# Kernel tuning notes

Measured on AMD Instinct MI355X. Metric: run time of the kernel, lower is better.

The kernel has to match this reference:

```python
import jax, jax.numpy as jnp
import numpy as np

HEADS = 8
DIM_HEAD = 64
QUERY_DIM = 512
CONTEXT_DIM = 768
INNER = HEADS * DIM_HEAD  # 512


def setup_inputs() -> dict:
    key = jax.random.key(0)
    ks = jax.random.split(key, 8)
    s = lambda fan_in: 1.0 / np.sqrt(fan_in)
    return {
        "x": jax.random.normal(ks[0], (16, 4096, QUERY_DIM), dtype=jnp.float32),
        "context": jax.random.normal(ks[1], (16, 77, CONTEXT_DIM), dtype=jnp.float32),
        "ln_gamma": jnp.ones((QUERY_DIM,), dtype=jnp.float32),
        "ln_beta": jnp.zeros((QUERY_DIM,), dtype=jnp.float32),
        "Wq": jax.random.uniform(ks[2], (QUERY_DIM, INNER), jnp.float32, -s(QUERY_DIM), s(QUERY_DIM)),
        "Wk": jax.random.uniform(ks[3], (CONTEXT_DIM, INNER), jnp.float32, -s(CONTEXT_DIM), s(CONTEXT_DIM)),
        "Wv": jax.random.uniform(ks[4], (CONTEXT_DIM, INNER), jnp.float32, -s(CONTEXT_DIM), s(CONTEXT_DIM)),
        "Wo": jax.random.uniform(ks[5], (INNER, QUERY_DIM), jnp.float32, -s(INNER), s(INNER)),
        "bo": jax.random.uniform(ks[6], (QUERY_DIM,), jnp.float32, -s(INNER), s(INNER)),
    }


def _layernorm(x, gamma, beta, eps=1e-5):
    mu = jnp.mean(x, axis=-1, keepdims=True)
    var = jnp.mean((x - mu) ** 2, axis=-1, keepdims=True)
    return (x - mu) * jax.lax.rsqrt(var + eps) * gamma + beta


def reference(x, context, ln_gamma, ln_beta, Wq, Wk, Wv, Wo, bo):
    B, N, D = x.shape
    scale = DIM_HEAD ** -0.5
    h = _layernorm(x, ln_gamma, ln_beta)
    # project then split heads: [B, H, S, d]
    q = (h @ Wq).reshape(B, N, HEADS, DIM_HEAD).transpose(0, 2, 1, 3)
    M = context.shape[1]
    k = (context @ Wk).reshape(B, M, HEADS, DIM_HEAD).transpose(0, 2, 1, 3)
    v = (context @ Wv).reshape(B, M, HEADS, DIM_HEAD).transpose(0, 2, 1, 3)
    scores = jnp.einsum("bhnd,bhmd->bhnm", q, k) * scale
    attn = jax.nn.softmax(scores, axis=-1)
    out = jnp.einsum("bhnm,bhmd->bhnd", attn, v)  # [B,H,N,d]
    out = out.transpose(0, 2, 1, 3).reshape(B, N, INNER)
    return x + out @ Wo + bo
```

## Files before the change

kernel.cpp:

```cpp
#include <hip/hip_runtime.h>


#define DQ 512
#define DC 768
#define MCTX 77
#define MPAD 96
#define DH 64

typedef __attribute__((ext_vector_type(8))) short bf16x8;
typedef __attribute__((ext_vector_type(4))) short s16x4;
typedef __attribute__((ext_vector_type(4))) float f32x4;
typedef __attribute__((ext_vector_type(16))) float f32x16;

__device__ __forceinline__ short f2bf(float f) {
    unsigned u = __builtin_bit_cast(unsigned, f);
    u = (u + 0x7FFFu + ((u >> 16) & 1u)) >> 16;
    return (short)u;
}
__device__ __forceinline__ unsigned cvtpk(float lo, float hi) {
    unsigned r;
    asm("v_cvt_pk_bf16_f32 %0, %1, %2" : "=v"(r) : "v"(lo), "v"(hi));
    return r;
}

#define SWZ(row, byte) ((byte) ^ (((row) & 7) << 4))
#define MFMA(a, b, c) __builtin_amdgcn_mfma_f32_16x16x32_bf16((a), (b), (c), 0, 0, 0)
#define MFMA32(a, b, c) __builtin_amdgcn_mfma_f32_32x32x16_bf16((a), (b), (c), 0, 0, 0)

__global__ void prep_weights(const float* __restrict__ Wq, const float* __restrict__ Wk,
                             const float* __restrict__ Wv, const float* __restrict__ Wo,
                             short* __restrict__ WqF, short* __restrict__ WkT,
                             short* __restrict__ WvT, short* __restrict__ WoF) {
    __shared__ float t[32][33];
    int bid = blockIdx.x;
    if (bid < 256) {
        const float* src = (bid < 128) ? Wq : Wo;
        short* dst = (bid < 128) ? WqF : WoF;
        int vb = bid & 127;
        int idx = vb * 256 + threadIdx.x;
        int lane = idx & 63;
        int chunk = idx >> 6;
        int tt = chunk % 16, ks = chunk / 16;
        int n = tt * 32 + (lane & 31);
        int k0 = ks * 16 + (lane >> 5) * 8;
        bf16x8 v;
#pragma unroll
        for (int j = 0; j < 8; ++j) v[j] = f2bf(src[(size_t)(k0 + j) * 512 + n]);
        *(bf16x8*)(dst + (size_t)idx * 8) = v;
    } else {
        const float* src = (bid < 640) ? Wk : Wv;
        short* dst = (bid < 640) ? WkT : WvT;
        int vb = (bid - 256) % 384;
        int tn = vb % 16, tk = vb / 16;
        int tx = threadIdx.x & 31, ty = threadIdx.x >> 5;
#pragma unroll
        for (int i = 0; i < 32; i += 8)
            t[ty + i][tx] = src[(size_t)(tk * 32 + ty + i) * 512 + tn * 32 + tx];
        __syncthreads();
#pragma unroll
        for (int i = 0; i < 32; i += 8)
            dst[(size_t)(tn * 32 + ty + i) * 768 + tk * 32 + tx] = f2bf(t[tx][ty + i]);
    }
}

__global__ __launch_bounds__(256, 1) void kv_proj(const float* __restrict__ ctxin,
                                                  const short* __restrict__ WkT,
                                                  const short* __restrict__ WvT,
                                                  short* __restrict__ Kb,
                                                  short* __restrict__ VbT) {
    int b = blockIdx.x >> 2;
    int kv = (blockIdx.x >> 1) & 1;
    int half = blockIdx.x & 1;
    const short* WT = kv ? WvT : WkT;

    __shared__ short A[48 * 768];
    const int tid = threadIdx.x;
    const int lane = tid & 63, wv = tid >> 6;
    const int l15 = lane & 15, l4 = lane >> 4;

#pragma unroll
    for (int it = 0; it < 36; ++it) {
        int id = it * 256 + tid;
        int row = id / 192, col = (id % 192) * 4;
        int gctx = half * 48 + row;
        float4 v = make_float4(0.f, 0.f, 0.f, 0.f);
        if (gctx < MCTX)
            v = ((const float4*)(ctxin + ((size_t)(b * MCTX + gctx)) * DC))[id % 192];
        s16x4 s4;
        s4[0] = f2bf(v.x); s4[1] = f2bf(v.y); s4[2] = f2bf(v.z); s4[3] = f2bf(v.w);
        *(s16x4*)((char*)A + row * 1536 + SWZ(row, col * 2)) = s4;
    }
    __syncthreads();

    f32x4 zf = {0.f, 0.f, 0.f, 0.f};
    f32x4 acc[3][8];
#pragma unroll
    for (int m = 0; m < 3; ++m)
#pragma unroll
        for (int nb = 0; nb < 8; ++nb) acc[m][nb] = zf;

    for (int ks = 0; ks < 24; ++ks) {
        bf16x8 bb[8], aa[3];
#pragma unroll
        for (int nb = 0; nb < 8; ++nb) {
            int n = wv * 128 + nb * 16 + l15;
            bb[nb] = *(const bf16x8*)((const char*)WT + (size_t)n * 1536 + ks * 64 + l4 * 16);
        }
#pragma unroll
        for (int m = 0; m < 3; ++m) {
            int row = m * 16 + l15;
            aa[m] = *(const bf16x8*)((char*)A + row * 1536 + SWZ(row, ks * 64 + l4 * 16));
        }
#pragma unroll
        for (int nb = 0; nb < 8; ++nb)
#pragma unroll
            for (int m = 0; m < 3; ++m) acc[m][nb] = MFMA(aa[m], bb[nb], acc[m][nb]);
    }

    if (kv == 0) {
#pragma unroll
        for (int m = 0; m < 3; ++m)
#pragma unroll
            for (int nb = 0; nb < 8; ++nb)
#pragma unroll
                for (int r = 0; r < 4; ++r) {
                    int ctxi = half * 48 + m * 16 + l4 * 4 + r;
                    int col = wv * 128 + nb * 16 + l15;
                    Kb[((size_t)(b * MPAD + ctxi)) * 512 + col] = f2bf(acc[m][nb][r]);
                }
    } else {
#pragma unroll
        for (int m = 0; m < 3; ++m)
#pragma unroll
            for (int nb = 0; nb < 8; ++nb)
#pragma unroll
                for (int r = 0; r < 4; ++r) {
                    int ctxi = half * 48 + m * 16 + l4 * 4 + r;
                    int col = wv * 128 + nb * 16 + l15;
                    VbT[((size_t)(b * 512 + col)) * MPAD + ctxi] = f2bf(acc[m][nb][r]);
                }
    }
}

__global__ __launch_bounds__(512, 4) void fused_attn(
    const float* __restrict__ x, const float* __restrict__ gamma,
    const float* __restrict__ beta, const short* __restrict__ WqF,
    const short* __restrict__ WoF, const short* __restrict__ Kb,
    const short* __restrict__ VbT, const float* __restrict__ bo,
    float* __restrict__ out) {
    __shared__ short A[64 * 512];

    const int tid = threadIdx.x;
    const int lane = tid & 63, wv = tid >> 6;
    const int l15 = lane & 15, l4 = lane >> 4;
    const int l31 = lane & 31, hi5 = lane >> 5;
    const int swz = (blockIdx.x & 7) * 128 + (blockIdx.x >> 3);
    const int b = swz >> 6;
    const size_t rowbase = (size_t)swz * 64;
    const int cb = wv * 64;

    {
        float g[8], be[8];
        float4 g0 = ((const float4*)gamma)[lane * 2], g1 = ((const float4*)gamma)[lane * 2 + 1];
        float4 b0 = ((const float4*)beta)[lane * 2], b1 = ((const float4*)beta)[lane * 2 + 1];
        g[0] = g0.x; g[1] = g0.y; g[2] = g0.z; g[3] = g0.w;
        g[4] = g1.x; g[5] = g1.y; g[6] = g1.z; g[7] = g1.w;
        be[0] = b0.x; be[1] = b0.y; be[2] = b0.z; be[3] = b0.w;
        be[4] = b1.x; be[5] = b1.y; be[6] = b1.z; be[7] = b1.w;
#pragma unroll 1
        for (int g4 = 0; g4 < 2; ++g4) {
            float4 v0[4], v1[4];
#pragma unroll
            for (int j = 0; j < 4; ++j) {
                int row = wv * 8 + g4 * 4 + j;
                const float4* xp = (const float4*)(x + (rowbase + row) * DQ);
                v0[j] = xp[lane * 2];
                v1[j] = xp[lane * 2 + 1];
            }
#pragma unroll
            for (int j = 0; j < 4; ++j) {
                int row = wv * 8 + g4 * 4 + j;
                float vv[8] = {v0[j].x, v0[j].y, v0[j].z, v0[j].w,
                               v1[j].x, v1[j].y, v1[j].z, v1[j].w};
                float s = 0.f, s2 = 0.f;
#pragma unroll
                for (int i = 0; i < 8; ++i) { s += vv[i]; s2 = fmaf(vv[i], vv[i], s2); }
#pragma unroll
                for (int m = 1; m < 64; m <<= 1) {
                    s += __shfl_xor(s, m);
                    s2 += __shfl_xor(s2, m);
                }
                float mu = s * (1.f / 512.f);
                float var = s2 * (1.f / 512.f) - mu * mu;
                float rs = rsqrtf(var + 1e-5f);
                float hn[8];
#pragma unroll
                for (int i = 0; i < 8; ++i) hn[i] = (vv[i] - mu) * rs * g[i] + be[i];
                uint4 hv = make_uint4(cvtpk(hn[0], hn[1]), cvtpk(hn[2], hn[3]),
                                      cvtpk(hn[4], hn[5]), cvtpk(hn[6], hn[7]));
                *(uint4*)((char*)A + row * 1024 + SWZ(row, lane * 16)) = hv;
            }
        }
    }

    f32x4 zf = {0.f, 0.f, 0.f, 0.f};

#define LDWF(dst, W, ks)                                                                   \
    _Pragma("unroll") for (int tt = 0; tt < 2; ++tt) {                                     \
        (dst)[tt] = *(const bf16x8*)((W) +                                                 \
            (size_t)((((ks)*16 + wv * 2 + tt) * 64 + lane)) * 8);                          \
    }
#define LDT32(dst, ks)                                                                     \
    _Pragma("unroll") for (int tt = 0; tt < 2; ++tt) {                                     \
        int row = tt * 32 + l31;                                                           \
        (dst)[tt] = *(const bf16x8*)((char*)A + row * 1024 +                               \
                                     SWZ(row, (ks)*32 + hi5 * 16));                        \
    }
#define GSTEP_Q(W, ACC, WBASE, kk)                                                         \
    {                                                                                      \
        bf16x8 hb[2];                                                                      \
        LDT32(hb, (kk));                                                                   \
        _Pragma("unroll") for (int mt = 0; mt < 2; ++mt)                                   \
            _Pragma("unroll") for (int nt = 0; nt < 2; ++nt)                               \
                ACC[mt][nt] = MFMA32((W)[mt], hb[nt], ACC[mt][nt]);                        \
        LDWF((W), (WBASE), (kk) + 4);                                                      \
    }
#define GSTEP_Q_NR(W, ACC, kk)                                                             \
    {                                                                                      \
        bf16x8 hb[2];                                                                      \
        LDT32(hb, (kk));                                                                   \
        _Pragma("unroll") for (int mt = 0; mt < 2; ++mt)                                   \
            _Pragma("unroll") for (int nt = 0; nt < 2; ++nt)                               \
                ACC[mt][nt] = MFMA32((W)[mt], hb[nt], ACC[mt][nt]);                        \
    }
#define GSTEP_O(W, ACC, WBASE, kk)                                                         \
    {                                                                                      \
        bf16x8 hb[2];                                                                      \
        LDT32(hb, (kk));                                                                   \
        _Pragma("unroll") for (int mt = 0; mt < 2; ++mt)                                   \
            _Pragma("unroll") for (int ct = 0; ct < 2; ++ct)                               \
                ACC[mt][ct] = MFMA32(hb[mt], (W)[ct], ACC[mt][ct]);                        \
        LDWF((W), (WBASE), (kk) + 4);                                                      \
    }
#define GSTEP_O_NR(W, ACC, kk)                                                             \
    {                                                                                      \
        bf16x8 hb[2];                                                                      \
        LDT32(hb, (kk));                                                                   \
        _Pragma("unroll") for (int mt = 0; mt < 2; ++mt)                                   \
            _Pragma("unroll") for (int ct = 0; ct < 2; ++ct)                               \
                ACC[mt][ct] = MFMA32(hb[mt], (W)[ct], ACC[mt][ct]);                        \
    }

    {
        bf16x8 w0[2], w1[2], w2[2], w3[2];
        LDWF(w0, WqF, 0);
        LDWF(w1, WqF, 1);
        LDWF(w2, WqF, 2);
        LDWF(w3, WqF, 3);
        __syncthreads();

        f32x16 qa[2][2];
#pragma unroll
        for (int mt = 0; mt < 2; ++mt)
#pragma unroll
            for (int nt = 0; nt < 2; ++nt)
#pragma unroll
                for (int i = 0; i < 16; ++i) qa[mt][nt][i] = 0.f;

#pragma unroll 1
        for (int ks = 0; ks < 28; ks += 4) {
            GSTEP_Q(w0, qa, WqF, ks)
            GSTEP_Q(w1, qa, WqF, ks + 1)
            GSTEP_Q(w2, qa, WqF, ks + 2)
            GSTEP_Q(w3, qa, WqF, ks + 3)
        }
        GSTEP_Q_NR(w0, qa, 28)
        GSTEP_Q_NR(w1, qa, 29)
        GSTEP_Q_NR(w2, qa, 30)
        GSTEP_Q_NR(w3, qa, 31)
        __syncthreads();

#pragma unroll
        for (int mt = 0; mt < 2; ++mt)
#pragma unroll
            for (int nt = 0; nt < 2; ++nt)
#pragma unroll
                for (int g = 0; g < 4; ++g) {
                    uint2 qv = make_uint2(
                        cvtpk(qa[mt][nt][g * 4] * 0.125f, qa[mt][nt][g * 4 + 1] * 0.125f),
                        cvtpk(qa[mt][nt][g * 4 + 2] * 0.125f, qa[mt][nt][g * 4 + 3] * 0.125f));
                    int row = nt * 32 + l31;
                    int colb = (cb + mt * 32 + 8 * g + 4 * hi5) * 2;
                    *(uint2*)((char*)A + row * 1024 + SWZ(row, colb)) = qv;
                }
    }

    {
        const int srcA = ((l4 & 1) << 5) + l15;
        const int srcB = srcA + 16;
        const bool hi = (l4 >> 1) != 0;

#pragma unroll 1
        for (int rp = 0; rp < 4; ++rp) {
            bf16x8 qf0, qf1;
            {
                int qrow = rp * 16 + l15;
                qf0 = *(const bf16x8*)((char*)A + qrow * 1024 + SWZ(qrow, cb * 2 + l4 * 16));
                qf1 = *(const bf16x8*)((char*)A + qrow * 1024 + SWZ(qrow, cb * 2 + 64 + l4 * 16));
            }
            f32x4 sc[5];
            __builtin_amdgcn_s_setprio(1);
#pragma unroll
            for (int f = 0; f < 5; ++f) {
                bf16x8 k0 = *(const bf16x8*)(Kb + ((size_t)(b * MPAD + f * 16 + l15)) * 512 +
                                             cb + l4 * 8);
                bf16x8 k1 = *(const bf16x8*)(Kb + ((size_t)(b * MPAD + f * 16 + l15)) * 512 +
                                             cb + 32 + l4 * 8);
                sc[f] = MFMA(k0, qf0, zf);
                sc[f] = MFMA(k1, qf1, sc[f]);
            }
            __builtin_amdgcn_s_setprio(0);
            float m = -1e30f;
#pragma unroll
            for (int f = 0; f < 5; ++f)
#pragma unroll
                for (int r = 0; r < 4; ++r) {
                    float v = sc[f][r];
                    if (f == 4 && (64 + l4 * 4 + r) >= MCTX) v = -1e30f;
                    sc[f][r] = v;
                    m = fmaxf(m, v);
                }
            m = fmaxf(m, __shfl_xor(m, 16));
            m = fmaxf(m, __shfl_xor(m, 32));
            float s = 0.f;
#pragma unroll
            for (int f = 0; f < 5; ++f)
#pragma unroll
                for (int r = 0; r < 4; ++r) {
                    float p = __expf(sc[f][r] - m);
                    sc[f][r] = p;
                    s += p;
                }
            s += __shfl_xor(s, 16);
            s += __shfl_xor(s, 32);
            float inv = 1.f / s;
            unsigned pk[6][2];
#pragma unroll
            for (int f = 0; f < 5; ++f) {
                pk[f][0] = cvtpk(sc[f][0] * inv, sc[f][1] * inv);
                pk[f][1] = cvtpk(sc[f][2] * inv, sc[f][3] * inv);
            }
            pk[5][0] = 0; pk[5][1] = 0;

            f32x4 ov[4];
#pragma unroll
            for (int nb = 0; nb < 4; ++nb) ov[nb] = zf;
#pragma unroll
            for (int ks = 0; ks < 3; ++ks) {
                unsigned aL0 = __shfl((int)pk[2 * ks][0], srcA);
                unsigned aL1 = __shfl((int)pk[2 * ks][1], srcA);
                unsigned aH0 = __shfl((int)pk[2 * ks + 1][0], srcA);
                unsigned aH1 = __shfl((int)pk[2 * ks + 1][1], srcA);
                unsigned bL0 = __shfl((int)pk[2 * ks][0], srcB);
                unsigned bL1 = __shfl((int)pk[2 * ks][1], srcB);
                unsigned bH0 = __shfl((int)pk[2 * ks + 1][0], srcB);
                unsigned bH1 = __shfl((int)pk[2 * ks + 1][1], srcB);
                unsigned paw[4];
                paw[0] = hi ? aH0 : aL0;
                paw[1] = hi ? aH1 : aL1;
                paw[2] = hi ? bH0 : bL0;
                paw[3] = hi ? bH1 : bL1;
                bf16x8 ap = __builtin_bit_cast(bf16x8, paw);
                __builtin_amdgcn_s_setprio(1);
#pragma unroll
                for (int nb = 0; nb < 4; ++nb) {
                    bf16x8 bv = *(const bf16x8*)(VbT +
                                                 ((size_t)(b * 512 + cb + nb * 16 + l15)) * MPAD +
                                                 ks * 32 + l4 * 8);
                    ov[nb] = MFMA(bv, ap, ov[nb]);
                }
                __builtin_amdgcn_s_setprio(0);
            }
#pragma unroll
            for (int nb = 0; nb < 4; ++nb) {
                uint2 av = make_uint2(cvtpk(ov[nb][0], ov[nb][1]),
                                      cvtpk(ov[nb][2], ov[nb][3]));
                int row = rp * 16 + l15;
                int colb = (cb + nb * 16 + l4 * 4) * 2;
                *(uint2*)((char*)A + row * 1024 + SWZ(row, colb)) = av;
            }
        }
    }

    {
        bf16x8 w0[2], w1[2], w2[2], w3[2];
        LDWF(w0, WoF, 0);
        LDWF(w1, WoF, 1);
        LDWF(w2, WoF, 2);
        LDWF(w3, WoF, 3);
        __syncthreads();

        f32x16 oa[2][2];
#pragma unroll
        for (int mt = 0; mt < 2; ++mt)
#pragma unroll
            for (int ct = 0; ct < 2; ++ct)
#pragma unroll
                for (int i = 0; i < 16; ++i) oa[mt][ct][i] = 0.f;

#pragma unroll 1
        for (int ks = 0; ks < 28; ks += 4) {
            GSTEP_O(w0, oa, WoF, ks)
            GSTEP_O(w1, oa, WoF, ks + 1)
            GSTEP_O(w2, oa, WoF, ks + 2)
            GSTEP_O(w3, oa, WoF, ks + 3)
        }
        GSTEP_O_NR(w0, oa, 28)
        GSTEP_O_NR(w1, oa, 29)
        GSTEP_O_NR(w2, oa, 30)
        GSTEP_O_NR(w3, oa, 31)

#pragma unroll
        for (int mt = 0; mt < 2; ++mt)
#pragma unroll
            for (int ct = 0; ct < 2; ++ct) {
                int col = cb + ct * 32 + l31;
                float bov = bo[col];
                float xv[16];
#pragma unroll
                for (int rg = 0; rg < 16; ++rg) {
                    int row = mt * 32 + (rg & 3) + 8 * (rg >> 2) + 4 * hi5;
                    xv[rg] = x[(rowbase + row) * DQ + col];
                }
#pragma unroll
                for (int rg = 0; rg < 16; ++rg) {
                    int row = mt * 32 + (rg & 3) + 8 * (rg >> 2) + 4 * hi5;
                    size_t gi = (rowbase + row) * DQ + col;
                    out[gi] = xv[rg] + oa[mt][ct][rg] + bov;
                }
            }
    }
}

extern "C" void kernel_launch(void* const* d_in, const int* in_sizes, int n_in,
                              void* d_out, int out_size, void* d_ws, size_t ws_size,
                              hipStream_t stream) {
    const float* x = (const float*)d_in[0];
    const float* ctx = (const float*)d_in[1];
    const float* gamma = (const float*)d_in[2];
    const float* beta = (const float*)d_in[3];
    const float* Wq = (const float*)d_in[4];
    const float* Wk = (const float*)d_in[5];
    const float* Wv = (const float*)d_in[6];
    const float* Wo = (const float*)d_in[7];
    const float* bo = (const float*)d_in[8];
    float* out = (float*)d_out;

    char* ws = (char*)d_ws;
    short* WqF = (short*)(ws + 0);
    short* WkT = (short*)(ws + 524288);
    short* WvT = (short*)(ws + 1310720);
    short* WoF = (short*)(ws + 2097152);
    short* Kb = (short*)(ws + 2621440);
    short* VbT = (short*)(ws + 4194304);

    prep_weights<<<1024, 256, 0, stream>>>(Wq, Wk, Wv, Wo, WqF, WkT, WvT, WoF);
    kv_proj<<<64, 256, 0, stream>>>(ctx, WkT, WvT, Kb, VbT);
    fused_attn<<<1024, 512, 0, stream>>>(x, gamma, beta, WqF, WoF, Kb, VbT, bo, out);
}
```

Baseline: 195.7 us.

## Process 128 rows per block with 16 waves to halve weight reloads

Each fused attention block now covers 128 query rows with 1024 threads instead of 64 rows with 512 threads. Each wave owns one 32-column slice of the Q and output projections across all 128 rows, so every weight fragment loaded from global memory is reused across twice as many rows and total weight traffic is halved. The attention stage splits the 16 waves into two groups of row pairs, and the Wo prefetch is moved ahead of the attention stage. The cost is double the LDS per block (128 KB), which allows fewer resident blocks per CU and larger synchronisation groups, and there are only 512 blocks to fill the GPU.

```diff
diff --git a/kernel.cpp b/kernel.cpp
--- a/kernel.cpp
+++ b/kernel.cpp
@@ -6,6 +6,7 @@
 #define MCTX 77
 #define MPAD 96
 #define DH 64
+#define ROWS 128
 
 typedef __attribute__((ext_vector_type(8))) short bf16x8;
 typedef __attribute__((ext_vector_type(4))) short s16x4;
@@ -142,22 +143,21 @@
     }
 }
 
-__global__ __launch_bounds__(512, 4) void fused_attn(
+__global__ __launch_bounds__(1024, 4) void fused_attn(
     const float* __restrict__ x, const float* __restrict__ gamma,
     const float* __restrict__ beta, const short* __restrict__ WqF,
     const short* __restrict__ WoF, const short* __restrict__ Kb,
     const short* __restrict__ VbT, const float* __restrict__ bo,
     float* __restrict__ out) {
-    __shared__ short A[64 * 512];
+    __shared__ short A[ROWS * 512];
 
     const int tid = threadIdx.x;
-    const int lane = tid & 63, wv = tid >> 6;
+    const int lane = tid & 63, w16 = tid >> 6;
     const int l15 = lane & 15, l4 = lane >> 4;
     const int l31 = lane & 31, hi5 = lane >> 5;
-    const int swz = (blockIdx.x & 7) * 128 + (blockIdx.x >> 3);
-    const int b = swz >> 6;
-    const size_t rowbase = (size_t)swz * 64;
-    const int cb = wv * 64;
+    const int swz = (blockIdx.x & 7) * 64 + (blockIdx.x >> 3);
+    const int b = swz >> 5;
+    const size_t rowbase = (size_t)swz * ROWS;
 
     {
         float g[8], be[8];
@@ -172,14 +172,14 @@
             float4 v0[4], v1[4];
 #pragma unroll
             for (int j = 0; j < 4; ++j) {
-                int row = wv * 8 + g4 * 4 + j;
+                int row = w16 * 8 + g4 * 4 + j;
                 const float4* xp = (const float4*)(x + (rowbase + row) * DQ);
                 v0[j] = xp[lane * 2];
                 v1[j] = xp[lane * 2 + 1];
             }
 #pragma unroll
             for (int j = 0; j < 4; ++j) {
-                int row = wv * 8 + g4 * 4 + j;
+                int row = w16 * 8 + g4 * 4 + j;
                 float vv[8] = {v0[j].x, v0[j].y, v0[j].z, v0[j].w,
                                v1[j].x, v1[j].y, v1[j].z, v1[j].w};
                 float s = 0.f, s2 = 0.f;
@@ -205,67 +205,58 @@
 
     f32x4 zf = {0.f, 0.f, 0.f, 0.f};
 
-#define LDWF(dst, W, ks)                                                                   \
-    _Pragma("unroll") for (int tt = 0; tt < 2; ++tt) {                                     \
-        (dst)[tt] = *(const bf16x8*)((W) +                                                 \
-            (size_t)((((ks)*16 + wv * 2 + tt) * 64 + lane)) * 8);                          \
-    }
-#define LDT32(dst, ks)                                                                     \
-    _Pragma("unroll") for (int tt = 0; tt < 2; ++tt) {                                     \
-        int row = tt * 32 + l31;                                                           \
-        (dst)[tt] = *(const bf16x8*)((char*)A + row * 1024 +                               \
+#define LDWF1(dst, W, ks)                                                                  \
+    (dst) = *(const bf16x8*)((W) + (size_t)((((ks)*16 + w16) * 64 + lane)) * 8);
+#define LDT128(dst, ks)                                                                    \
+    _Pragma("unroll") for (int nt = 0; nt < 4; ++nt) {                                     \
+        int row = nt * 32 + l31;                                                           \
+        (dst)[nt] = *(const bf16x8*)((char*)A + row * 1024 +                               \
                                      SWZ(row, (ks)*32 + hi5 * 16));                        \
     }
 #define GSTEP_Q(W, ACC, WBASE, kk)                                                         \
     {                                                                                      \
-        bf16x8 hb[2];                                                                      \
-        LDT32(hb, (kk));                                                                   \
-        _Pragma("unroll") for (int mt = 0; mt < 2; ++mt)                                   \
-            _Pragma("unroll") for (int nt = 0; nt < 2; ++nt)                               \
-                ACC[mt][nt] = MFMA32((W)[mt], hb[nt], ACC[mt][nt]);                        \
-        LDWF((W), (WBASE), (kk) + 4);                                                      \
+        bf16x8 hb[4];                                                                      \
+        LDT128(hb, (kk));                                                                  \
+        _Pragma("unroll") for (int nt = 0; nt < 4; ++nt)                                   \
+            ACC[nt] = MFMA32((W), hb[nt], ACC[nt]);                                        \
+        LDWF1((W), (WBASE), (kk) + 4);                                                     \
     }
 #define GSTEP_Q_NR(W, ACC, kk)                                                             \
     {                                                                                      \
-        bf16x8 hb[2];                                                                      \
-        LDT32(hb, (kk));                                                                   \
-        _Pragma("unroll") for (int mt = 0; mt < 2; ++mt)                                   \
-            _Pragma("unroll") for (int nt = 0; nt < 2; ++nt)                               \
-                ACC[mt][nt] = MFMA32((W)[mt], hb[nt], ACC[mt][nt]);                        \
+        bf16x8 hb[4];                                                                      \
+        LDT128(hb, (kk));                                                                  \
+        _Pragma("unroll") for (int nt = 0; nt < 4; ++nt)                                   \
+            ACC[nt] = MFMA32((W), hb[nt], ACC[nt]);                                        \
     }
 #define GSTEP_O(W, ACC, WBASE, kk)                                                         \
     {                                                                                      \
-        bf16x8 hb[2];                                                                      \
-        LDT32(hb, (kk));                                                                   \
-        _Pragma("unroll") for (int mt = 0; mt < 2; ++mt)                                   \
-            _Pragma("unroll") for (int ct = 0; ct < 2; ++ct)                               \
-                ACC[mt][ct] = MFMA32(hb[mt], (W)[ct], ACC[mt][ct]);                        \
-        LDWF((W), (WBASE), (kk) + 4);                                                      \
+        bf16x8 hb[4];                                                                      \
+        LDT128(hb, (kk));                                                                  \
+        _Pragma("unroll") for (int mt = 0; mt < 4; ++mt)                                   \
+            ACC[mt] = MFMA32(hb[mt], (W), ACC[mt]);                                        \
+        LDWF1((W), (WBASE), (kk) + 4);                                                     \
     }
 #define GSTEP_O_NR(W, ACC, kk)                                                             \
     {                                                                                      \
-        bf16x8 hb[2];                                                                      \
-        LDT32(hb, (kk));                                                                   \
-        _Pragma("unroll") for (int mt = 0; mt < 2; ++mt)                                   \
-            _Pragma("unroll") for (int ct = 0; ct < 2; ++ct)                               \
-                ACC[mt][ct] = MFMA32(hb[mt], (W)[ct], ACC[mt][ct]);                        \
+        bf16x8 hb[4];                                                                      \
+        LDT128(hb, (kk));                                                                  \
+        _Pragma("unroll") for (int mt = 0; mt < 4; ++mt)                                   \
+            ACC[mt] = MFMA32(hb[mt], (W), ACC[mt]);                                        \
     }
 
     {
-        bf16x8 w0[2], w1[2], w2[2], w3[2];
-        LDWF(w0, WqF, 0);
-        LDWF(w1, WqF, 1);
-        LDWF(w2, WqF, 2);
-        LDWF(w3, WqF, 3);
+        bf16x8 w0, w1, w2, w3;
+        LDWF1(w0, WqF, 0);
+        LDWF1(w1, WqF, 1);
+        LDWF1(w2, WqF, 2);
+        LDWF1(w3, WqF, 3);
         __syncthreads();
 
-        f32x16 qa[2][2];
-#pragma unroll
-        for (int mt = 0; mt < 2; ++mt)
-#pragma unroll
-            for (int nt = 0; nt < 2; ++nt)
-#pragma unroll
-                for (int i = 0; i < 16; ++i) qa[mt][nt][i] = 0.f;
+        f32x16 qa[4];
+#pragma unroll
+        for (int nt = 0; nt < 4; ++nt)
+#pragma unroll
+            for (int i = 0; i < 16; ++i) qa[nt][i] = 0.f;
 
 #pragma unroll 1
         for (int ks = 0; ks < 28; ks += 4) {
@@ -281,27 +272,35 @@
         __syncthreads();
 
 #pragma unroll
-        for (int mt = 0; mt < 2; ++mt)
-#pragma unroll
-            for (int nt = 0; nt < 2; ++nt)
-#pragma unroll
-                for (int g = 0; g < 4; ++g) {
-                    uint2 qv = make_uint2(
-                        cvtpk(qa[mt][nt][g * 4] * 0.125f, qa[mt][nt][g * 4 + 1] * 0.125f),
-                        cvtpk(qa[mt][nt][g * 4 + 2] * 0.125f, qa[mt][nt][g * 4 + 3] * 0.125f));
-                    int row = nt * 32 + l31;
-                    int colb = (cb + mt * 32 + 8 * g + 4 * hi5) * 2;
-                    *(uint2*)((char*)A + row * 1024 + SWZ(row, colb)) = qv;
-                }
-    }
+        for (int nt = 0; nt < 4; ++nt)
+#pragma unroll
+            for (int g = 0; g < 4; ++g) {
+                uint2 qv = make_uint2(
+                    cvtpk(qa[nt][g * 4] * 0.125f, qa[nt][g * 4 + 1] * 0.125f),
+                    cvtpk(qa[nt][g * 4 + 2] * 0.125f, qa[nt][g * 4 + 3] * 0.125f));
+                int row = nt * 32 + l31;
+                int colb = (w16 * 32 + 8 * g + 4 * hi5) * 2;
+                *(uint2*)((char*)A + row * 1024 + SWZ(row, colb)) = qv;
+            }
+        __syncthreads();
+    }
+
+    bf16x8 wo0, wo1, wo2, wo3;
+    LDWF1(wo0, WoF, 0);
+    LDWF1(wo1, WoF, 1);
+    LDWF1(wo2, WoF, 2);
+    LDWF1(wo3, WoF, 3);
 
     {
+        const int cb = (w16 & 7) * 64;
+        const int rpb = (w16 >> 3) * 4;
         const int srcA = ((l4 & 1) << 5) + l15;
         const int srcB = srcA + 16;
         const bool hi = (l4 >> 1) != 0;
 
 #pragma unroll 1
-        for (int rp = 0; rp < 4; ++rp) {
+        for (int rp2 = 0; rp2 < 4; ++rp2) {
+            const int rp = rpb + rp2;
             bf16x8 qf0, qf1;
             {
                 int qrow = rp * 16 + l15;
@@ -393,39 +392,31 @@
     }
 
     {
-        bf16x8 w0[2], w1[2], w2[2], w3[2];
-        LDWF(w0, WoF, 0);
-        LDWF(w1, WoF, 1);
-        LDWF(w2, WoF, 2);
-        LDWF(w3, WoF, 3);
         __syncthreads();
 
-        f32x16 oa[2][2];
-#pragma unroll
-        for (int mt = 0; mt < 2; ++mt)
-#pragma unroll
-            for (int ct = 0; ct < 2; ++ct)
-#pragma unroll
-                for (int i = 0; i < 16; ++i) oa[mt][ct][i] = 0.f;
+        f32x16 oa[4];
+#pragma unroll
+        for (int mt = 0; mt < 4; ++mt)
+#pragma unroll
+            for (int i = 0; i < 16; ++i) oa[mt][i] = 0.f;
 
 #pragma unroll 1
         for (int ks = 0; ks < 28; ks += 4) {
-            GSTEP_O(w0, oa, WoF, ks)
-            GSTEP_O(w1, oa, WoF, ks + 1)
-            GSTEP_O(w2, oa, WoF, ks + 2)
-            GSTEP_O(w3, oa, WoF, ks + 3)
-        }
-        GSTEP_O_NR(w0, oa, 28)
-        GSTEP_O_NR(w1, oa, 29)
-        GSTEP_O_NR(w2, oa, 30)
-        GSTEP_O_NR(w3, oa, 31)
-
-#pragma unroll
-        for (int mt = 0; mt < 2; ++mt)
-#pragma unroll
-            for (int ct = 0; ct < 2; ++ct) {
-                int col = cb + ct * 32 + l31;
-                float bov = bo[col];
+            GSTEP_O(wo0, oa, WoF, ks)
+            GSTEP_O(wo1, oa, WoF, ks + 1)
+            GSTEP_O(wo2, oa, WoF, ks + 2)
+            GSTEP_O(wo3, oa, WoF, ks + 3)
+        }
+        GSTEP_O_NR(wo0, oa, 28)
+        GSTEP_O_NR(wo1, oa, 29)
+        GSTEP_O_NR(wo2, oa, 30)
+        GSTEP_O_NR(wo3, oa, 31)
+
+        {
+            int col = w16 * 32 + l31;
+            float bov = bo[col];
+#pragma unroll
+            for (int mt = 0; mt < 4; ++mt) {
                 float xv[16];
 #pragma unroll
                 for (int rg = 0; rg < 16; ++rg) {
@@ -436,9 +427,10 @@
                 for (int rg = 0; rg < 16; ++rg) {
                     int row = mt * 32 + (rg & 3) + 8 * (rg >> 2) + 4 * hi5;
                     size_t gi = (rowbase + row) * DQ + col;
-                    out[gi] = xv[rg] + oa[mt][ct][rg] + bov;
-                }
-            }
+                    out[gi] = xv[rg] + oa[mt][rg] + bov;
+                }
+            }
+        }
     }
 }
 
@@ -466,5 +458,5 @@
 
     prep_weights<<<1024, 256, 0, stream>>>(Wq, Wk, Wv, Wo, WqF, WkT, WvT, WoF);
     kv_proj<<<64, 256, 0, stream>>>(ctx, WkT, WvT, Kb, VbT);
-    fused_attn<<<1024, 512, 0, stream>>>(x, gamma, beta, WqF, WoF, Kb, VbT, bo, out);
-}
+    fused_attn<<<512, 1024, 0, stream>>>(x, gamma, beta, WqF, WoF, Kb, VbT, bo, out);
+}
```

After: 190.7 us. 1.03x faster.

## Retile Q and O projections to 32-row by 128-col warp tiles

Applied to the files above, without the earlier changes.

Changes the per-warp tiling of the Q and output projection GEMMs from a 64x64 tile (2x2 of 32x32 MFMAs) to a 32x128 tile (one A row-block times four weight column-blocks). This halves the LDS reads of activations per MFMA, doubles the per-warp weight fragment loads from global memory, and shortens weight prefetch to two stages. The Q writeback to LDS now happens before the barrier rather than after it, which removes one synchronisation, and the setprio scope in the PV loop is widened to cover all k-steps. The trade-off is more global and L2 weight traffic per block in exchange for less LDS pressure.

```diff
diff --git a/kernel.cpp b/kernel.cpp
--- a/kernel.cpp
+++ b/kernel.cpp
@@ -154,10 +154,10 @@
     const int lane = tid & 63, wv = tid >> 6;
     const int l15 = lane & 15, l4 = lane >> 4;
     const int l31 = lane & 31, hi5 = lane >> 5;
+    const int rg = wv >> 2, cg = wv & 3;
     const int swz = (blockIdx.x & 7) * 128 + (blockIdx.x >> 3);
     const int b = swz >> 6;
     const size_t rowbase = (size_t)swz * 64;
-    const int cb = wv * 64;
 
     {
         float g[8], be[8];
@@ -205,97 +205,84 @@
 
     f32x4 zf = {0.f, 0.f, 0.f, 0.f};
 
-#define LDWF(dst, W, ks)                                                                   \
-    _Pragma("unroll") for (int tt = 0; tt < 2; ++tt) {                                     \
+#define LDWF4(dst, W, ks)                                                                  \
+    _Pragma("unroll") for (int tt = 0; tt < 4; ++tt) {                                     \
         (dst)[tt] = *(const bf16x8*)((W) +                                                 \
-            (size_t)((((ks)*16 + wv * 2 + tt) * 64 + lane)) * 8);                          \
-    }
-#define LDT32(dst, ks)                                                                     \
-    _Pragma("unroll") for (int tt = 0; tt < 2; ++tt) {                                     \
-        int row = tt * 32 + l31;                                                           \
-        (dst)[tt] = *(const bf16x8*)((char*)A + row * 1024 +                               \
-                                     SWZ(row, (ks)*32 + hi5 * 16));                        \
-    }
-#define GSTEP_Q(W, ACC, WBASE, kk)                                                         \
+            (size_t)((((ks)*16 + cg * 4 + tt) * 64 + lane)) * 8);                          \
+    }
+#define LDT1R(dst, ks)                                                                     \
     {                                                                                      \
-        bf16x8 hb[2];                                                                      \
-        LDT32(hb, (kk));                                                                   \
-        _Pragma("unroll") for (int mt = 0; mt < 2; ++mt)                                   \
-            _Pragma("unroll") for (int nt = 0; nt < 2; ++nt)                               \
-                ACC[mt][nt] = MFMA32((W)[mt], hb[nt], ACC[mt][nt]);                        \
-        LDWF((W), (WBASE), (kk) + 4);                                                      \
-    }
-#define GSTEP_Q_NR(W, ACC, kk)                                                             \
+        int row_ = rg * 32 + l31;                                                          \
+        (dst) = *(const bf16x8*)((char*)A + row_ * 1024 +                                  \
+                                 SWZ(row_, (ks)*32 + hi5 * 16));                           \
+    }
+#define GSTEPQ(W, kk)                                                                      \
     {                                                                                      \
-        bf16x8 hb[2];                                                                      \
-        LDT32(hb, (kk));                                                                   \
-        _Pragma("unroll") for (int mt = 0; mt < 2; ++mt)                                   \
-            _Pragma("unroll") for (int nt = 0; nt < 2; ++nt)                               \
-                ACC[mt][nt] = MFMA32((W)[mt], hb[nt], ACC[mt][nt]);                        \
-    }
-#define GSTEP_O(W, ACC, WBASE, kk)                                                         \
+        bf16x8 hb;                                                                         \
+        LDT1R(hb, (kk));                                                                   \
+        _Pragma("unroll") for (int ct = 0; ct < 4; ++ct)                                   \
+            qa[ct] = MFMA32((W)[ct], hb, qa[ct]);                                          \
+        LDWF4((W), WqF, (kk) + 2);                                                         \
+    }
+#define GSTEPQ_NR(W, kk)                                                                   \
     {                                                                                      \
-        bf16x8 hb[2];                                                                      \
-        LDT32(hb, (kk));                                                                   \
-        _Pragma("unroll") for (int mt = 0; mt < 2; ++mt)                                   \
-            _Pragma("unroll") for (int ct = 0; ct < 2; ++ct)                               \
-                ACC[mt][ct] = MFMA32(hb[mt], (W)[ct], ACC[mt][ct]);                        \
-        LDWF((W), (WBASE), (kk) + 4);                                                      \
-    }
-#define GSTEP_O_NR(W, ACC, kk)                                                             \
+        bf16x8 hb;                                                                         \
+        LDT1R(hb, (kk));                                                                   \
+        _Pragma("unroll") for (int ct = 0; ct < 4; ++ct)                                   \
+            qa[ct] = MFMA32((W)[ct], hb, qa[ct]);                                          \
+    }
+#define GSTEPO(W, kk)                                                                      \
     {                                                                                      \
-        bf16x8 hb[2];                                                                      \
-        LDT32(hb, (kk));                                                                   \
-        _Pragma("unroll") for (int mt = 0; mt < 2; ++mt)                                   \
-            _Pragma("unroll") for (int ct = 0; ct < 2; ++ct)                               \
-                ACC[mt][ct] = MFMA32(hb[mt], (W)[ct], ACC[mt][ct]);                        \
+        bf16x8 ab;                                                                         \
+        LDT1R(ab, (kk));                                                                   \
+        _Pragma("unroll") for (int ct = 0; ct < 4; ++ct)                                   \
+            oa[ct] = MFMA32(ab, (W)[ct], oa[ct]);                                          \
+        LDWF4((W), WoF, (kk) + 2);                                                         \
+    }
+#define GSTEPO_NR(W, kk)                                                                   \
+    {                                                                                      \
+        bf16x8 ab;                                                                         \
+        LDT1R(ab, (kk));                                                                   \
+        _Pragma("unroll") for (int ct = 0; ct < 4; ++ct)                                   \
+            oa[ct] = MFMA32(ab, (W)[ct], oa[ct]);                                          \
     }
 
     {
-        bf16x8 w0[2], w1[2], w2[2], w3[2];
-        LDWF(w0, WqF, 0);
-        LDWF(w1, WqF, 1);
-        LDWF(w2, WqF, 2);
-        LDWF(w3, WqF, 3);
+        bf16x8 wA[4], wB[4];
+        LDWF4(wA, WqF, 0);
+        LDWF4(wB, WqF, 1);
         __syncthreads();
 
-        f32x16 qa[2][2];
-#pragma unroll
-        for (int mt = 0; mt < 2; ++mt)
-#pragma unroll
-            for (int nt = 0; nt < 2; ++nt)
-#pragma unroll
-                for (int i = 0; i < 16; ++i) qa[mt][nt][i] = 0.f;
+        f32x16 qa[4];
+#pragma unroll
+        for (int ct = 0; ct < 4; ++ct)
+#pragma unroll
+            for (int i = 0; i < 16; ++i) qa[ct][i] = 0.f;
 
 #pragma unroll 1
-        for (int ks = 0; ks < 28; ks += 4) {
-            GSTEP_Q(w0, qa, WqF, ks)
-            GSTEP_Q(w1, qa, WqF, ks + 1)
-            GSTEP_Q(w2, qa, WqF, ks + 2)
-            GSTEP_Q(w3, qa, WqF, ks + 3)
-        }
-        GSTEP_Q_NR(w0, qa, 28)
-        GSTEP_Q_NR(w1, qa, 29)
-        GSTEP_Q_NR(w2, qa, 30)
-        GSTEP_Q_NR(w3, qa, 31)
+        for (int ks = 0; ks < 30; ks += 2) {
+            GSTEPQ(wA, ks)
+            GSTEPQ(wB, ks + 1)
+        }
+        GSTEPQ_NR(wA, 30)
+        GSTEPQ_NR(wB, 31)
+
+#pragma unroll
+        for (int ct = 0; ct < 4; ++ct)
+#pragma unroll
+            for (int g = 0; g < 4; ++g) {
+                uint2 qv = make_uint2(
+                    cvtpk(qa[ct][g * 4] * 0.125f, qa[ct][g * 4 + 1] * 0.125f),
+                    cvtpk(qa[ct][g * 4 + 2] * 0.125f, qa[ct][g * 4 + 3] * 0.125f));
+                int row = rg * 32 + l31;
+                int colb = (cg * 128 + ct * 32 + 8 * g + 4 * hi5) * 2;
+                *(uint2*)((char*)A + row * 1024 + SWZ(row, colb)) = qv;
+            }
         __syncthreads();
-
-#pragma unroll
-        for (int mt = 0; mt < 2; ++mt)
-#pragma unroll
-            for (int nt = 0; nt < 2; ++nt)
-#pragma unroll
-                for (int g = 0; g < 4; ++g) {
-                    uint2 qv = make_uint2(
-                        cvtpk(qa[mt][nt][g * 4] * 0.125f, qa[mt][nt][g * 4 + 1] * 0.125f),
-                        cvtpk(qa[mt][nt][g * 4 + 2] * 0.125f, qa[mt][nt][g * 4 + 3] * 0.125f));
-                    int row = nt * 32 + l31;
-                    int colb = (cb + mt * 32 + 8 * g + 4 * hi5) * 2;
-                    *(uint2*)((char*)A + row * 1024 + SWZ(row, colb)) = qv;
-                }
     }
 
     {
+        const int cb = wv * 64;
         const int srcA = ((l4 & 1) << 5) + l15;
         const int srcB = srcA + 16;
         const bool hi = (l4 >> 1) != 0;
@@ -355,6 +342,7 @@
             f32x4 ov[4];
 #pragma unroll
             for (int nb = 0; nb < 4; ++nb) ov[nb] = zf;
+            __builtin_amdgcn_s_setprio(1);
 #pragma unroll
             for (int ks = 0; ks < 3; ++ks) {
                 unsigned aL0 = __shfl((int)pk[2 * ks][0], srcA);
@@ -371,7 +359,6 @@
                 paw[2] = hi ? bH0 : bL0;
                 paw[3] = hi ? bH1 : bL1;
                 bf16x8 ap = __builtin_bit_cast(bf16x8, paw);
-                __builtin_amdgcn_s_setprio(1);
 #pragma unroll
                 for (int nb = 0; nb < 4; ++nb) {
                     bf16x8 bv = *(const bf16x8*)(VbT +
@@ -379,8 +366,8 @@
                                                  ks * 32 + l4 * 8);
                     ov[nb] = MFMA(bv, ap, ov[nb]);
                 }
-                __builtin_amdgcn_s_setprio(0);
-            }
+            }
+            __builtin_amdgcn_s_setprio(0);
 #pragma unroll
             for (int nb = 0; nb < 4; ++nb) {
                 uint2 av = make_uint2(cvtpk(ov[nb][0], ov[nb][1]),
@@ -393,52 +380,42 @@
     }
 
     {
-        bf16x8 w0[2], w1[2], w2[2], w3[2];
-        LDWF(w0, WoF, 0);
-        LDWF(w1, WoF, 1);
-        LDWF(w2, WoF, 2);
-        LDWF(w3, WoF, 3);
+        bf16x8 wA[4], wB[4];
+        LDWF4(wA, WoF, 0);
+        LDWF4(wB, WoF, 1);
         __syncthreads();
 
-        f32x16 oa[2][2];
-#pragma unroll
-        for (int mt = 0; mt < 2; ++mt)
-#pragma unroll
-            for (int ct = 0; ct < 2; ++ct)
-#pragma unroll
-                for (int i = 0; i < 16; ++i) oa[mt][ct][i] = 0.f;
+        f32x16 oa[4];
+#pragma unroll
+        for (int ct = 0; ct < 4; ++ct)
+#pragma unroll
+            for (int i = 0; i < 16; ++i) oa[ct][i] = 0.f;
 
 #pragma unroll 1
-        for (int ks = 0; ks < 28; ks += 4) {
-            GSTEP_O(w0, oa, WoF, ks)
-            GSTEP_O(w1, oa, WoF, ks + 1)
-            GSTEP_O(w2, oa, WoF, ks + 2)
-            GSTEP_O(w3, oa, WoF, ks + 3)
-        }
-        GSTEP_O_NR(w0, oa, 28)
-        GSTEP_O_NR(w1, oa, 29)
-        GSTEP_O_NR(w2, oa, 30)
-        GSTEP_O_NR(w3, oa, 31)
-
-#pragma unroll
-        for (int mt = 0; mt < 2; ++mt)
-#pragma unroll
-            for (int ct = 0; ct < 2; ++ct) {
-                int col = cb + ct * 32 + l31;
-                float bov = bo[col];
-                float xv[16];
-#pragma unroll
-                for (int rg = 0; rg < 16; ++rg) {
-                    int row = mt * 32 + (rg & 3) + 8 * (rg >> 2) + 4 * hi5;
-                    xv[rg] = x[(rowbase + row) * DQ + col];
-                }
-#pragma unroll
-                for (int rg = 0; rg < 16; ++rg) {
-                    int row = mt * 32 + (rg & 3) + 8 * (rg >> 2) + 4 * hi5;
-                    size_t gi = (rowbase + row) * DQ + col;
-                    out[gi] = xv[rg] + oa[mt][ct][rg] + bov;
-                }
-            }
+        for (int ks = 0; ks < 30; ks += 2) {
+            GSTEPO(wA, ks)
+            GSTEPO(wB, ks + 1)
+        }
+        GSTEPO_NR(wA, 30)
+        GSTEPO_NR(wB, 31)
+
+#pragma unroll
+        for (int ct = 0; ct < 4; ++ct) {
+            int col = cg * 128 + ct * 32 + l31;
+            float bov = bo[col];
+            float xv[16];
+#pragma unroll
+            for (int rgi = 0; rgi < 16; ++rgi) {
+                int row = rg * 32 + (rgi & 3) + 8 * (rgi >> 2) + 4 * hi5;
+                xv[rgi] = x[(rowbase + row) * DQ + col];
+            }
+#pragma unroll
+            for (int rgi = 0; rgi < 16; ++rgi) {
+                int row = rg * 32 + (rgi & 3) + 8 * (rgi >> 2) + 4 * hi5;
+                size_t gi = (rowbase + row) * DQ + col;
+                out[gi] = xv[rgi] + oa[ct][rgi] + bov;
+            }
+        }
     }
 }
 
```

Result: slower. 233.9 us (+19.5%).
